# Kernel tuning notes

Measured on AMD Instinct MI355X. Metric: run time of the kernel, lower is better.

Reference implementation:

```python
import jax, jax.numpy as jnp
import numpy as np

BATCH = 8192
NUM_VARS = 128
HID = 64
NUM_PARAMS = 2


def setup_inputs() -> dict:
    key = jax.random.key(0)
    ks = jax.random.split(key, 7)
    s = 0.1  # keep activations in a sane range
    return {
        "x": jax.random.normal(ks[0], (BATCH, NUM_VARS), jnp.float32),
        "w0": jax.random.normal(ks[1], (NUM_VARS, HID, NUM_VARS), jnp.float32) * s,
        "b0": jax.random.normal(ks[2], (NUM_VARS, HID), jnp.float32) * s,
        "w1": jax.random.normal(ks[3], (NUM_VARS, HID, HID), jnp.float32) * s,
        "b1": jax.random.normal(ks[4], (NUM_VARS, HID), jnp.float32) * s,
        "w2": jax.random.normal(ks[5], (NUM_VARS, NUM_PARAMS, HID), jnp.float32) * s,
        "b2": jax.random.normal(ks[6], (NUM_VARS, NUM_PARAMS), jnp.float32) * s,
    }


def reference(x, w0, b0, w1, b1, w2, b2):
    # adjacency = ones - eye (no self-loops), constant buffer in the torch model
    d = x.shape[1]
    adj = jnp.ones((d, d), x.dtype) - jnp.eye(d, dtype=x.dtype)  # [j, t]
    # layer 0: per-node masked linear over all other variables
    # torch: einsum('tij,ljt,bj->bti', w0, adj[None], x) + b0
    h = jnp.einsum('tij,jt,bj->bti', w0, adj, x) + b0  # [B, t=num_vars, hid]
    h = jax.nn.leaky_relu(h)  # negative_slope=0.01, matches F.leaky_relu
    # layer 1: per-node linear
    h = jnp.einsum('tij,btj->bti', w1, h) + b1
    h = jax.nn.leaky_relu(h)
    # output layer (no activation)
    out = jnp.einsum('tij,btj->bti', w2, h) + b2  # [B, num_vars, num_params]
    # torch returns torch.unbind(out, 1); we return the stacked equivalent
    return out
```

## Files before the change

### kernel.cpp

```cpp
#include <hip/hip_runtime.h>
#include <hip/hip_bf16.h>

typedef __attribute__((ext_vector_type(8))) short short8;
typedef __attribute__((ext_vector_type(16))) float f32x16;
typedef __attribute__((ext_vector_type(2))) unsigned uint2v;

#define LEAK 0.01f

__device__ __forceinline__ f32x16 mfma32(short8 a, short8 b, f32x16 c) {
    return __builtin_amdgcn_mfma_f32_32x32x16_bf16(a, b, c, 0, 0, 0);
}
__device__ __forceinline__ unsigned pkbf(float a, float b) {
    __hip_bfloat162 t = __float22bfloat162_rn(make_float2(a, b));
    return *reinterpret_cast<unsigned*>(&t);
}

#if defined(__has_builtin) && __has_builtin(__builtin_amdgcn_permlane32_swap)
__device__ __forceinline__ void plswap(unsigned &a, unsigned &b, int ) {
    uint2v r = __builtin_amdgcn_permlane32_swap(a, b, false, false);
    a = r.x; b = r.y;
}
#else
__device__ __forceinline__ void plswap(unsigned &a, unsigned &b, int h) {
    unsigned ax = (unsigned)__shfl_xor((int)a, 32);
    unsigned bx = (unsigned)__shfl_xor((int)b, 32);
    unsigned na = h ? bx : a;
    unsigned nb = h ? b  : ax;
    a = na; b = nb;
}
#endif

__device__ __forceinline__ void transition(const f32x16 &A0, const f32x16 &A1,
                                           short8 out[4], int h) {
    unsigned pk[2][8];
    #pragma unroll
    for (int nt = 0; nt < 2; ++nt) {
        const f32x16 &A = nt ? A1 : A0;
        #pragma unroll
        for (int s = 0; s < 8; ++s) {
            float u = A[2*s], v = A[2*s+1];
            u = fmaxf(u, LEAK * u); v = fmaxf(v, LEAK * v);
            pk[nt][s] = pkbf(u, v);
        }
    }
    #pragma unroll
    for (int ks = 0; ks < 4; ++ks) {
        const int nt = ks >> 1, ss = (ks & 1) * 4;
        unsigned d0 = pk[nt][ss], d1 = pk[nt][ss+1], d2 = pk[nt][ss+2], d3 = pk[nt][ss+3];
        plswap(d0, d2, h);
        plswap(d1, d3, h);
        union { unsigned u[4]; short8 s; } U;
        U.u[0] = d0; U.u[1] = d1; U.u[2] = d2; U.u[3] = d3;
        out[ks] = U.s;
    }
}

__global__ __launch_bounds__(256) void prep_kernel(
    const float* __restrict__ x,  const float* __restrict__ w0, const float* __restrict__ b0,
    const float* __restrict__ w1, const float* __restrict__ b1,
    const float* __restrict__ w2, const float* __restrict__ b2,
    __hip_bfloat16* __restrict__ xp,  __hip_bfloat16* __restrict__ w0p,
    __hip_bfloat16* __restrict__ w1p, __hip_bfloat16* __restrict__ w2p)
{
    const int idx = blockIdx.x * 256 + threadIdx.x;
    float v[8];
    #pragma unroll
    for (int e = 0; e < 8; ++e) v[e] = 0.f;
    __hip_bfloat16* dst;

    if (idx < 147456) {
        int b = idx / 18, ch = idx - b * 18;
        dst = xp + b * 144 + ch * 8;
        if (ch < 16) {
            const float* s = x + b * 128 + ch * 8;
            #pragma unroll
            for (int e = 0; e < 8; ++e) v[e] = s[e];
        } else if (ch == 16) v[0] = 1.f;
    } else if (idx < 294912) {
        int i = idx - 147456;
        int r = i / 18, ch = i - r * 18;
        int t = r >> 6;
        dst = w0p + r * 144 + ch * 8;
        if (ch < 16) {
            const float* s = w0 + r * 128 + ch * 8;
            #pragma unroll
            for (int e = 0; e < 8; ++e) v[e] = s[e];
            if ((t >> 3) == ch) v[t & 7] = 0.f;
        } else if (ch == 16) v[0] = b0[r];
    } else if (idx < 376832) {
        int i = idx - 294912;
        int r = i / 10, ch = i - r * 10;
        dst = w1p + r * 80 + ch * 8;
        if (ch < 8) {
            const float* s = w1 + r * 64 + ch * 8;
            #pragma unroll
            for (int e = 0; e < 8; ++e) v[e] = s[e];
        } else if (ch == 8) v[0] = b1[r];
    } else {
        int i = idx - 376832;
        int r = i / 10, ch = i - r * 10;
        int t = r >> 5, n = r & 31;
        dst = w2p + r * 80 + ch * 8;
        if (n < 2) {
            if (ch < 8) {
                const float* s = w2 + (t * 2 + n) * 64 + ch * 8;
                #pragma unroll
                for (int e = 0; e < 8; ++e) v[e] = s[e];
            } else if (ch == 8) v[0] = b2[t * 2 + n];
        }
    }
    union { unsigned u[4]; short8 s; } U;
    #pragma unroll
    for (int p = 0; p < 4; ++p) U.u[p] = pkbf(v[2*p], v[2*p+1]);
    *reinterpret_cast<short8*>(dst) = U.s;
}

__global__ __launch_bounds__(256, 2) void mlp_kernel(
    const __hip_bfloat16* __restrict__ xp,
    const __hip_bfloat16* __restrict__ w0p,
    const __hip_bfloat16* __restrict__ w1p,
    const __hip_bfloat16* __restrict__ w2p,
    float* __restrict__ dst, int direct)
{
    const int tid  = threadIdx.x;
    const int wave = tid >> 6;
    const int lane = tid & 63;
    const int h    = lane >> 5;
    const int c    = lane & 31;

    const int bid   = blockIdx.x;
    const int t     = (bid & 7) * 16 + ((bid >> 3) & 15);
    const int chunk = bid >> 7;
    const int rb0   = chunk * 1024 + wave * 256;

    const __hip_bfloat16* xr0 = xp + (rb0 + c) * 144 + h * 8;
    short8 xf[9];
    #pragma unroll
    for (int ks = 0; ks < 9; ++ks)
        xf[ks] = *reinterpret_cast<const short8*>(xr0 + ks * 16);

    const __hip_bfloat16* w0t = w0p + t * 9216;
    const __hip_bfloat16* w1t = w1p + t * 5120;
    const __hip_bfloat16* w2t = w2p + t * 2560;
    short8 w0f[2][9], w1f[2][5], w2f[5];
    #pragma unroll
    for (int nt = 0; nt < 2; ++nt)
        #pragma unroll
        for (int ks = 0; ks < 9; ++ks)
            w0f[nt][ks] = *reinterpret_cast<const short8*>(w0t + (nt*32 + c)*144 + ks*16 + h*8);
    #pragma unroll
    for (int nt = 0; nt < 2; ++nt)
        #pragma unroll
        for (int ks = 0; ks < 5; ++ks)
            w1f[nt][ks] = *reinterpret_cast<const short8*>(w1t + (nt*32 + c)*80 + ks*16 + h*8);
    #pragma unroll
    for (int ks = 0; ks < 5; ++ks)
        w2f[ks] = *reinterpret_cast<const short8*>(w2t + c*80 + ks*16 + h*8);

    union { unsigned u[4]; short8 s; } OneU;
    OneU.u[0] = (h == 0) ? 0x00003f80u : 0u;
    OneU.u[1] = 0u; OneU.u[2] = 0u; OneU.u[3] = 0u;
    const short8 onef = OneU.s;

    f32x16 ZV;
    #pragma unroll
    for (int i = 0; i < 16; ++i) ZV[i] = 0.f;

    #pragma unroll
    for (int tile = 0; tile < 8; ++tile) {
        const int brow = rb0 + tile * 32 + c;

        short8 xn[9];
        if (tile < 7) {
            const __hip_bfloat16* xr = xr0 + (tile + 1) * (32 * 144);
            #pragma unroll
            for (int ks = 0; ks < 9; ++ks)
                xn[ks] = *reinterpret_cast<const short8*>(xr + ks * 16);
        }

        f32x16 acc0a, acc0b;
        __builtin_amdgcn_s_setprio(1);
        acc0a = mfma32(w0f[0][0], xf[0], ZV);
        acc0b = mfma32(w0f[1][0], xf[0], ZV);
        #pragma unroll
        for (int ks = 1; ks < 9; ++ks) {
            acc0a = mfma32(w0f[0][ks], xf[ks], acc0a);
            acc0b = mfma32(w0f[1][ks], xf[ks], acc0b);
        }
        __builtin_amdgcn_s_setprio(0);

        short8 h1f[4];
        transition(acc0a, acc0b, h1f, h);

        f32x16 acc1a, acc1b;
        __builtin_amdgcn_s_setprio(1);
        acc1a = mfma32(w1f[0][0], h1f[0], ZV);
        acc1b = mfma32(w1f[1][0], h1f[0], ZV);
        #pragma unroll
        for (int ks = 1; ks < 4; ++ks) {
            acc1a = mfma32(w1f[0][ks], h1f[ks], acc1a);
            acc1b = mfma32(w1f[1][ks], h1f[ks], acc1b);
        }
        acc1a = mfma32(w1f[0][4], onef, acc1a);
        acc1b = mfma32(w1f[1][4], onef, acc1b);
        __builtin_amdgcn_s_setprio(0);

        short8 h2f[4];
        transition(acc1a, acc1b, h2f, h);

        f32x16 acc2;
        __builtin_amdgcn_s_setprio(1);
        acc2 = mfma32(w2f[0], h2f[0], ZV);
        #pragma unroll
        for (int ks = 1; ks < 4; ++ks) acc2 = mfma32(w2f[ks], h2f[ks], acc2);
        acc2 = mfma32(w2f[4], onef, acc2);
        __builtin_amdgcn_s_setprio(0);

        if (h == 0) {
            float2 v = make_float2(acc2[0], acc2[1]);
            if (direct) *reinterpret_cast<float2*>(dst + brow * 256 + t * 2) = v;
            else        *reinterpret_cast<float2*>(dst + t * 16384 + brow * 2) = v;
        }

        #pragma unroll
        for (int ks = 0; ks < 9; ++ks) xf[ks] = xn[ks];
    }
}

__global__ __launch_bounds__(256) void transpose_kernel(
    const float* __restrict__ tmp, float* __restrict__ out)
{
    __shared__ float tile[32][257];
    const int b0 = blockIdx.x * 32;
    const int tid = threadIdx.x;
    #pragma unroll
    for (int it = 0; it < 16; ++it) {
        int idx = it * 256 + tid;
        int tt = idx >> 5, r = idx & 31;
        float2 v = *reinterpret_cast<const float2*>(tmp + tt * 16384 + (b0 + r) * 2);
        tile[r][tt * 2]     = v.x;
        tile[r][tt * 2 + 1] = v.y;
    }
    __syncthreads();
    #pragma unroll
    for (int r = 0; r < 32; ++r)
        out[(b0 + r) * 256 + tid] = tile[r][tid];
}

extern "C" void kernel_launch(void* const* d_in, const int* in_sizes, int n_in,
                              void* d_out, int out_size, void* d_ws, size_t ws_size,
                              hipStream_t stream)
{
    const float* x  = (const float*)d_in[0];
    const float* w0 = (const float*)d_in[1];
    const float* b0 = (const float*)d_in[2];
    const float* w1 = (const float*)d_in[3];
    const float* b1 = (const float*)d_in[4];
    const float* w2 = (const float*)d_in[5];
    const float* b2 = (const float*)d_in[6];
    float* out = (float*)d_out;

    const size_t OFF_W0  = 2359296;
    const size_t OFF_W1  = OFF_W0 + 2359296;
    const size_t OFF_W2  = OFF_W1 + 1310720;
    const size_t OFF_TMP = OFF_W2 + 655360;
    const size_t NEED_TMP = OFF_TMP + 8388608;

    if (ws_size < OFF_TMP) return;

    char* ws = (char*)d_ws;
    __hip_bfloat16* xp  = (__hip_bfloat16*)(ws);
    __hip_bfloat16* w0p = (__hip_bfloat16*)(ws + OFF_W0);
    __hip_bfloat16* w1p = (__hip_bfloat16*)(ws + OFF_W1);
    __hip_bfloat16* w2p = (__hip_bfloat16*)(ws + OFF_W2);
    float* tmp = (float*)(ws + OFF_TMP);

    const int use_tmp = (ws_size >= NEED_TMP) ? 1 : 0;
    float* dstp = use_tmp ? tmp : out;

    prep_kernel<<<1632, 256, 0, stream>>>(x, w0, b0, w1, b1, w2, b2, xp, w0p, w1p, w2p);
    mlp_kernel<<<1024, 256, 0, stream>>>(xp, w0p, w1p, w2p, dstp, use_tmp ? 0 : 1);
    if (use_tmp)
        transpose_kernel<<<256, 256, 0, stream>>>(tmp, out);
}
```

Before: 119.4 us.

## Stage layer-1/2 weights in LDS and shorten x prefetch lifetime

Moves the per-node w1 and w2 weight fragments out of registers into shared memory. They are loaded cooperatively once per block and reread from LDS for each tile, with an opaque offset so the compiler does not hoist those reads back into registers. The x prefetch for the next tile now overwrites xf after the layer-0 MFMAs instead of using a separate xn buffer. Together these cut register pressure, which may let more waves stay resident, but every tile now pays LDS reads and the block has a barrier and less load latency to hide.

New measurement: 123.0 us. +3.0%, slower.

```diff
diff --git a/kernel.cpp b/kernel.cpp
--- a/kernel.cpp
+++ b/kernel.cpp
@@ -122,6 +122,8 @@
     const __hip_bfloat16* __restrict__ w2p,
     float* __restrict__ dst, int direct)
 {
+    __shared__ __align__(16) char sW[15360];
+
     const int tid  = threadIdx.x;
     const int wave = tid >> 6;
     const int lane = tid & 63;
@@ -133,6 +135,19 @@
     const int chunk = bid >> 7;
     const int rb0   = chunk * 1024 + wave * 256;
 
+    const __hip_bfloat16* w1t = w1p + t * 5120;
+    const __hip_bfloat16* w2t = w2p + t * 2560;
+    {
+        const short8* g1 = reinterpret_cast<const short8*>(w1t);
+        const short8* g2 = reinterpret_cast<const short8*>(w2t);
+        #pragma unroll
+        for (int it = 0; it < 4; ++it) {
+            int i = tid + it * 256;
+            if (i < 640)      *reinterpret_cast<short8*>(sW + i * 16) = g1[i];
+            else if (i < 960) *reinterpret_cast<short8*>(sW + i * 16) = g2[i - 640];
+        }
+    }
+
     const __hip_bfloat16* xr0 = xp + (rb0 + c) * 144 + h * 8;
     short8 xf[9];
     #pragma unroll
@@ -140,22 +155,12 @@
         xf[ks] = *reinterpret_cast<const short8*>(xr0 + ks * 16);
 
     const __hip_bfloat16* w0t = w0p + t * 9216;
-    const __hip_bfloat16* w1t = w1p + t * 5120;
-    const __hip_bfloat16* w2t = w2p + t * 2560;
-    short8 w0f[2][9], w1f[2][5], w2f[5];
+    short8 w0f[2][9];
     #pragma unroll
     for (int nt = 0; nt < 2; ++nt)
         #pragma unroll
         for (int ks = 0; ks < 9; ++ks)
             w0f[nt][ks] = *reinterpret_cast<const short8*>(w0t + (nt*32 + c)*144 + ks*16 + h*8);
-    #pragma unroll
-    for (int nt = 0; nt < 2; ++nt)
-        #pragma unroll
-        for (int ks = 0; ks < 5; ++ks)
-            w1f[nt][ks] = *reinterpret_cast<const short8*>(w1t + (nt*32 + c)*80 + ks*16 + h*8);
-    #pragma unroll
-    for (int ks = 0; ks < 5; ++ks)
-        w2f[ks] = *reinterpret_cast<const short8*>(w2t + c*80 + ks*16 + h*8);
 
     union { unsigned u[4]; short8 s; } OneU;
     OneU.u[0] = (h == 0) ? 0x00003f80u : 0u;
@@ -166,17 +171,15 @@
     #pragma unroll
     for (int i = 0; i < 16; ++i) ZV[i] = 0.f;
 
+    __syncthreads();
+
     #pragma unroll
     for (int tile = 0; tile < 8; ++tile) {
         const int brow = rb0 + tile * 32 + c;
 
-        short8 xn[9];
-        if (tile < 7) {
-            const __hip_bfloat16* xr = xr0 + (tile + 1) * (32 * 144);
-            #pragma unroll
-            for (int ks = 0; ks < 9; ++ks)
-                xn[ks] = *reinterpret_cast<const short8*>(xr + ks * 16);
-        }
+        unsigned inv = 0;
+        asm volatile("" : "+v"(inv));
+        const char* sWt = sW + inv;
 
         f32x16 acc0a, acc0b;
         __builtin_amdgcn_s_setprio(1);
@@ -189,20 +192,26 @@
         }
         __builtin_amdgcn_s_setprio(0);
 
+        if (tile < 7) {
+            const __hip_bfloat16* xr = xr0 + (tile + 1) * (32 * 144);
+            #pragma unroll
+            for (int ks = 0; ks < 9; ++ks)
+                xf[ks] = *reinterpret_cast<const short8*>(xr + ks * 16);
+        }
+
         short8 h1f[4];
         transition(acc0a, acc0b, h1f, h);
 
         f32x16 acc1a, acc1b;
         __builtin_amdgcn_s_setprio(1);
-        acc1a = mfma32(w1f[0][0], h1f[0], ZV);
-        acc1b = mfma32(w1f[1][0], h1f[0], ZV);
-        #pragma unroll
-        for (int ks = 1; ks < 4; ++ks) {
-            acc1a = mfma32(w1f[0][ks], h1f[ks], acc1a);
-            acc1b = mfma32(w1f[1][ks], h1f[ks], acc1b);
-        }
-        acc1a = mfma32(w1f[0][4], onef, acc1a);
-        acc1b = mfma32(w1f[1][4], onef, acc1b);
+        #pragma unroll
+        for (int ks = 0; ks < 5; ++ks) {
+            short8 wa = *reinterpret_cast<const short8*>(sWt + c*160 + ks*32 + h*16);
+            short8 wb = *reinterpret_cast<const short8*>(sWt + (32 + c)*160 + ks*32 + h*16);
+            short8 bf = (ks < 4) ? h1f[ks] : onef;
+            if (ks == 0) { acc1a = mfma32(wa, bf, ZV);    acc1b = mfma32(wb, bf, ZV); }
+            else         { acc1a = mfma32(wa, bf, acc1a); acc1b = mfma32(wb, bf, acc1b); }
+        }
         __builtin_amdgcn_s_setprio(0);
 
         short8 h2f[4];
@@ -210,10 +219,12 @@
 
         f32x16 acc2;
         __builtin_amdgcn_s_setprio(1);
-        acc2 = mfma32(w2f[0], h2f[0], ZV);
-        #pragma unroll
-        for (int ks = 1; ks < 4; ++ks) acc2 = mfma32(w2f[ks], h2f[ks], acc2);
-        acc2 = mfma32(w2f[4], onef, acc2);
+        #pragma unroll
+        for (int ks = 0; ks < 5; ++ks) {
+            short8 wv = *reinterpret_cast<const short8*>(sWt + 10240 + c*160 + ks*32 + h*16);
+            short8 bf = (ks < 4) ? h2f[ks] : onef;
+            acc2 = (ks == 0) ? mfma32(wv, bf, ZV) : mfma32(wv, bf, acc2);
+        }
         __builtin_amdgcn_s_setprio(0);
 
         if (h == 0) {
@@ -221,9 +232,6 @@
             if (direct) *reinterpret_cast<float2*>(dst + brow * 256 + t * 2) = v;
             else        *reinterpret_cast<float2*>(dst + t * 16384 + brow * 2) = v;
         }
-
-        #pragma unroll
-        for (int ks = 0; ks < 9; ++ks) xf[ks] = xn[ks];
     }
 }
 
```
